# Kernel tuning notes

Hardware: AMD Instinct MI355X
Metric: run time of the kernel (lower is better)

The kernel has to match this reference:

```python
import jax, jax.numpy as jnp
import numpy as np

N = 50000   # nodes
E = 600000  # edges per edge_index
G = 64      # graphs in batch
H = 128     # hidden_neurons == n_node_features
EPS = 1e-12 # F.normalize eps


def sage(x, edge, Wl, bl, Wr, norm):
    # PyG SAGEConv (aggr='mean'): out_i = lin_l(mean_{j->i} x_j) + lin_r(x_i)
    src, dst = edge[0], edge[1]
    s = jax.ops.segment_sum(x[src], dst, num_segments=N)          # [N,H]
    cnt = jax.ops.segment_sum(jnp.ones((edge.shape[1],), x.dtype), dst, num_segments=N)
    agg = s / jnp.maximum(cnt, 1.0)[:, None]
    out = agg @ Wl + bl + x @ Wr
    if norm:  # F.normalize(out, p=2, dim=-1)
        n = jnp.linalg.norm(out, axis=-1, keepdims=True)
        out = out / jnp.maximum(n, EPS)
    return out


def setup_inputs() -> dict:
    key = jax.random.key(0)
    ks = jax.random.split(key, 40)
    sc = 1.0 / np.sqrt(H)
    d = {}
    d["x"] = jax.random.normal(ks[0], (N, H), jnp.float32)
    d["eic"] = jax.random.randint(ks[1], (2, E), 0, N, dtype=jnp.int32)
    d["eid"] = jax.random.randint(ks[2], (2, E), 0, N, dtype=jnp.int32)
    d["eit"] = jax.random.randint(ks[3], (2, E), 0, N, dtype=jnp.int32)
    d["batch"] = jnp.sort(jax.random.randint(ks[4], (N,), 0, G, dtype=jnp.int32))
    i = 5
    for c in ["c1", "c2", "c3", "c4", "c5"]:
        d[c + "_Wl"] = jax.random.normal(ks[i], (H, H), jnp.float32) * sc; i += 1
        d[c + "_bl"] = jnp.zeros((H,), jnp.float32)
        d[c + "_Wr"] = jax.random.normal(ks[i], (H, H), jnp.float32) * sc; i += 1
    d["l0_W"] = jax.random.normal(ks[i], (H, H), jnp.float32) * sc; i += 1
    d["l0_b"] = jnp.zeros((H,), jnp.float32)
    d["l1_W"] = jax.random.normal(ks[i], (H, H), jnp.float32) * sc; i += 1
    d["l1_b"] = jnp.zeros((H,), jnp.float32)
    d["head_W"] = jax.random.normal(ks[i], (H, 1), jnp.float32) * sc; i += 1
    d["head_b"] = jnp.zeros((1,), jnp.float32)
    return d


def reference(x, eic, eid, eit, batch,
              c1_Wl, c1_bl, c1_Wr, c2_Wl, c2_bl, c2_Wr, c3_Wl, c3_bl, c3_Wr,
              c4_Wl, c4_bl, c4_Wr, c5_Wl, c5_bl, c5_Wr,
              l0_W, l0_b, l1_W, l1_b, head_W, head_b):
    h = sage(x, eid, c1_Wl, c1_bl, c1_Wr, True)
    for _ in range(2):  # it_b4_dest, shared conv2 weights
        h = sage(h, eic, c2_Wl, c2_bl, c2_Wr, True)
    h = sage(h, eit, c3_Wl, c3_bl, c3_Wr, False)  # conv3 normalize=False
    h = sage(h, eid, c4_Wl, c4_bl, c4_Wr, True)
    for _ in range(2):  # it_aft_dest, shared conv5 weights
        h = sage(h, eic, c5_Wl, c5_bl, c5_Wr, True)
    g = jax.ops.segment_sum(h, batch, num_segments=G)  # global_add_pool -> [G,H]
    g = jax.nn.relu(g @ l0_W + l0_b)
    g = jax.nn.relu(g @ l1_W + l1_b)
    return g @ head_W + head_b  # [G,1]
```

## Files before the change

kernel.cpp:

```cpp
#include <hip/hip_runtime.h>
#include <hip/hip_bf16.h>


constexpr int N_NODES = 50000;
constexpr int NE      = 600000;
constexpr int H       = 128;
constexpr int NG      = 64;
constexpr int N3      = 3 * N_NODES;

constexpr int NB   = (N3 + 1023) >> 10;
constexpr int EPB  = 2048;
constexpr int BPS  = (NE + EPB - 1) / EPB;
constexpr int CAP2 = 19456;

typedef __attribute__((ext_vector_type(8))) short short8;
typedef __attribute__((ext_vector_type(4))) float f32x4;

__device__ __forceinline__ ushort f2bf(float f) {
    uint x = __float_as_uint(f);
    return (ushort)((x + 0x7FFFu + ((x >> 16) & 1u)) >> 16);
}
__device__ __forceinline__ float bf2f(ushort u) {
    return __uint_as_float(((uint)u) << 16);
}


__global__ __launch_bounds__(256) void k_bucketize(
    const int* __restrict__ e0, const int* __restrict__ e1,
    const int* __restrict__ e2, int* __restrict__ gcnt,
    int* __restrict__ rcnt, int2* __restrict__ bucket) {
    __shared__ int hist[NB];
    __shared__ int basearr[NB];
    __shared__ int cur[NB];
    __shared__ int gposs[NB];
    __shared__ int2 stage[EPB];
    __shared__ int dstoff[EPB];

    int t = threadIdx.x;
    int s = blockIdx.x / BPS;
    int w = blockIdx.x - s * BPS;
    const int* ep = (s == 0 ? e0 : (s == 1 ? e1 : e2));
    int eBase = w * EPB;
    int m = NE - eBase;
    if (m > EPB) m = EPB;

    for (int i = t; i < NB; i += 256) hist[i] = 0;
    __syncthreads();

    int myk[EPB / 256], mys[EPB / 256];
#pragma unroll
    for (int k = 0; k < EPB / 256; ++k) {
        int i = t + 256 * k;
        if (i < m) {
            int d   = ep[NE + eBase + i];
            int src = ep[eBase + i];
            int key = s * N_NODES + d;
            myk[k] = key; mys[k] = src;
            atomicAdd(&hist[key >> 10], 1);
        } else {
            myk[k] = -1;
        }
    }
    __syncthreads();

    if (t == 0) {
        int run = 0;
        for (int b = 0; b < NB; ++b) { basearr[b] = run; run += hist[b]; }
    }
    __syncthreads();

    if (t < NB) {
        int h = hist[t];
        int p = (h + 7) & ~7;
        gposs[t] = p ? atomicAdd(&gcnt[t], p) : 0;
        if (h) atomicAdd(&rcnt[t], h);
        cur[t] = 0;
    }
    __syncthreads();

#pragma unroll
    for (int k = 0; k < EPB / 256; ++k) {
        if (myk[k] >= 0) {
            int b  = myk[k] >> 10;
            int sl = atomicAdd(&cur[b], 1);
            int p  = basearr[b] + sl;
            stage[p]  = make_int2(myk[k], mys[k]);
            dstoff[p] = b * CAP2 + gposs[b] + sl;
        }
    }
    __syncthreads();

    for (int i = t; i < m; i += 256) bucket[dstoff[i]] = stage[i];
    for (int i = t; i < NB * 8; i += 256) {
        int b = i >> 3, j = i & 7;
        int h = hist[b];
        int p = (h + 7) & ~7;
        if (h + j < p)
            bucket[(size_t)b * CAP2 + gposs[b] + h + j] = make_int2(-1, 0);
    }
}


__global__ __launch_bounds__(512) void k_scatter2(const int2* __restrict__ bucket,
                                                  const int* __restrict__ gcnt,
                                                  const int* __restrict__ rcnt,
                                                  int* __restrict__ ptr,
                                                  int* __restrict__ adj) {
    int b = blockIdx.x;
    int base = b << 10;
    int nk = N3 - base;
    if (nk > 1024) nk = 1024;
    __shared__ int lh[1024];
    __shared__ int lsum[512];
    __shared__ int lfill[1024];
    __shared__ int bb;
    int t = threadIdx.x;

    int rv = (t < NB) ? rcnt[t] : 0;
    lsum[t] = rv;
    __syncthreads();
    for (int off = 1; off < 512; off <<= 1) {
        int u = (t >= off) ? lsum[t - off] : 0;
        __syncthreads();
        if (t >= off) lsum[t] += u;
        __syncthreads();
    }
    if (t == b) bb = lsum[t] - rv;
    if (b == 0 && t == 0) ptr[N3] = 3 * NE;
    for (int i = t; i < 1024; i += 512) lh[i] = 0;
    __syncthreads();

    int c = gcnt[b];
    const int2* seg = bucket + (size_t)b * CAP2;
    for (int i = t; i < c; i += 512) {
        int k = seg[i].x;
        if (k >= 0) atomicAdd(&lh[k - base], 1);
    }
    __syncthreads();
    int v0 = lh[t * 2], v1 = lh[t * 2 + 1];
    int ts = v0 + v1;
    lsum[t] = ts;
    __syncthreads();
    for (int off = 1; off < 512; off <<= 1) {
        int u = (t >= off) ? lsum[t - off] : 0;
        __syncthreads();
        if (t >= off) lsum[t] += u;
        __syncthreads();
    }
    int ex = lsum[t] - ts + bb;
    int e0 = ex, e1 = ex + v0;
    if (t * 2     < nk) { ptr[base + t * 2]     = e0; lfill[t * 2]     = e0; }
    if (t * 2 + 1 < nk) { ptr[base + t * 2 + 1] = e1; lfill[t * 2 + 1] = e1; }
    __syncthreads();
    for (int i = t; i < c; i += 512) {
        int2 ed = seg[i];
        if (ed.x >= 0) {
            int pos = atomicAdd(&lfill[ed.x - base], 1);
            adj[pos] = ed.y;
        }
    }
}


__global__ void k_prep(int* __restrict__ zmem,
                       const float* W0l, const float* W0r, const float* W1l,
                       const float* W1r, const float* W2l, const float* W2r,
                       const float* W3l, const float* W3r, const float* W4l,
                       const float* W4r, ushort* __restrict__ Bpk) {
    int bid = blockIdx.x;
    int t   = threadIdx.x;
    if (bid < 640) {
        int idx = bid * 256 + t;
        if (idx >= 5 * 32768) return;
        int c = idx >> 15, r = idx & 32767;
        const float* Wl = (c == 0 ? W0l : c == 1 ? W1l : c == 2 ? W2l : c == 3 ? W3l : W4l);
        const float* Wr = (c == 0 ? W0r : c == 1 ? W1r : c == 2 ? W2r : c == 3 ? W3r : W4r);
        int n = r & 255, k = r >> 8;
        float w = (n < H) ? Wl[k * H + n] : Wr[k * H + (n - H)];
        int q = k >> 5, g = (k >> 3) & 3, j = k & 7;
        int off = ((q * 4 + g) * 256 + n) * 8 + j;
        ushort h = f2bf(w);
        ushort* bh = Bpk + (size_t)c * 65536;
        bh[off]         = h;
        bh[32768 + off] = f2bf(w - bf2f(h));
        return;
    }
    int tid = (bid - 640) * 256 + t;
    if (tid < NG * H + 2 * NB) zmem[tid] = 0;
}


__global__ __launch_bounds__(256) void k_gemm0(
    const float* __restrict__ x,
    const ushort* __restrict__ Bh, const ushort* __restrict__ Bl,
    ushort* __restrict__ z, ushort* __restrict__ yb) {
    __shared__ ushort Ash[2][64][136];
    int t = threadIdx.x;
    int rowBase = blockIdx.x * 64;
    {
        int row = t >> 2;
        int cs  = (t & 3) * 32;
        int grow = rowBase + row;
        if (grow > N_NODES - 1) grow = N_NODES - 1;
        const float4* src = (const float4*)(x + (size_t)grow * H + cs);
        ushort* dh = &Ash[0][row][cs];
        ushort* dl = &Ash[1][row][cs];
#pragma unroll
        for (int i = 0; i < 8; ++i) {
            float4 v = src[i];
            ushort4 hh, ll;
            hh.x = f2bf(v.x); ll.x = f2bf(v.x - bf2f(hh.x));
            hh.y = f2bf(v.y); ll.y = f2bf(v.y - bf2f(hh.y));
            hh.z = f2bf(v.z); ll.z = f2bf(v.z - bf2f(hh.z));
            hh.w = f2bf(v.w); ll.w = f2bf(v.w - bf2f(hh.w));
            *(ushort4*)(dh + i * 4) = hh;
            *(ushort4*)(dl + i * 4) = ll;
        }
    }
    __syncthreads();

    int wave = t >> 6, lane = t & 63;
    int m16 = lane & 15, q4 = lane >> 4;
    int n0 = wave * 64;

    f32x4 acc[4][4];
#pragma unroll
    for (int r = 0; r < 4; ++r)
#pragma unroll
        for (int c = 0; c < 4; ++c) {
            acc[r][c][0] = 0.f; acc[r][c][1] = 0.f;
            acc[r][c][2] = 0.f; acc[r][c][3] = 0.f;
        }

    for (int q = 0; q < 4; ++q) {
        short8 bh_[4], bl_[4], ah_[4], al_[4];
#pragma unroll
        for (int c = 0; c < 4; ++c) {
            int boff = ((q * 4 + q4) * 256 + n0 + c * 16 + m16) * 8;
            bh_[c] = *(const short8*)(Bh + boff);
            bl_[c] = *(const short8*)(Bl + boff);
        }
#pragma unroll
        for (int r = 0; r < 4; ++r) {
            ah_[r] = *(const short8*)&Ash[0][r * 16 + m16][q * 32 + q4 * 8];
            al_[r] = *(const short8*)&Ash[1][r * 16 + m16][q * 32 + q4 * 8];
        }
#pragma unroll
        for (int r = 0; r < 4; ++r)
#pragma unroll
            for (int c = 0; c < 4; ++c) {
                acc[r][c] = __builtin_amdgcn_mfma_f32_16x16x32_bf16(
                    ah_[r], bh_[c], acc[r][c], 0, 0, 0);
                acc[r][c] = __builtin_amdgcn_mfma_f32_16x16x32_bf16(
                    ah_[r], bl_[c], acc[r][c], 0, 0, 0);
                acc[r][c] = __builtin_amdgcn_mfma_f32_16x16x32_bf16(
                    al_[r], bh_[c], acc[r][c], 0, 0, 0);
            }
    }

#pragma unroll
    for (int r = 0; r < 4; ++r)
#pragma unroll
        for (int c = 0; c < 4; ++c) {
            int col = n0 + c * 16 + m16;
            ushort* op = (col < H) ? (z + col) : (yb + (col - H));
#pragma unroll
            for (int j = 0; j < 4; ++j) {
                int gr = rowBase + r * 16 + q4 * 4 + j;
                if (gr < N_NODES) op[(size_t)gr * H] = f2bf(acc[r][c][j]);
            }
        }
}


__global__ __launch_bounds__(512, 6) void k_fused2(
    const ushort* __restrict__ zin, const ushort* __restrict__ yin,
    ushort* __restrict__ zout, ushort* __restrict__ yout,
    const int* __restrict__ ptr, const int* __restrict__ adj,
    const float* __restrict__ bl,
    const ushort* __restrict__ Bh, const ushort* __restrict__ Blw,
    int norm) {
    __shared__ ushort Ash[2][32][136];
    int t = threadIdx.x;
    int rowBase = blockIdx.x * 32;
    int sl  = t & 15;
    int row = t >> 4;

    {
        int node = rowBase + row;
        if (node > N_NODES - 1) node = N_NODES - 1;
        int beg = ptr[node], end = ptr[node + 1];
        int deg = end - beg;
        const ushort* zrow = zin + sl * 8;
        float a[8];
#pragma unroll
        for (int k = 0; k < 8; ++k) a[k] = 0.f;

        for (int base = 0; base < deg; base += 16) {
            int m = deg - base;
            if (m > 16) m = 16;
            int idx = (sl < m) ? adj[beg + base + sl] : 0;
#pragma unroll
            for (int half = 0; half < 2; ++half) {
                int mh = m - half * 8;
                if (mh <= 0) continue;
                if (mh > 8) mh = 8;
                int hb = half * 8;
                short8 v[8];
#pragma unroll
                for (int jj = 0; jj < 8; ++jj) {
                    int nj = __shfl(idx, hb + jj, 16);
                    if (jj < mh) v[jj] = *(const short8*)(zrow + (size_t)nj * H);
                }
                if (mh == 8) {
#pragma unroll
                    for (int k = 0; k < 8; ++k)
                        a[k] += ((bf2f((ushort)v[0][k]) + bf2f((ushort)v[1][k])) +
                                 (bf2f((ushort)v[2][k]) + bf2f((ushort)v[3][k]))) +
                                ((bf2f((ushort)v[4][k]) + bf2f((ushort)v[5][k])) +
                                 (bf2f((ushort)v[6][k]) + bf2f((ushort)v[7][k])));
                } else if (mh >= 4) {
#pragma unroll
                    for (int k = 0; k < 8; ++k)
                        a[k] += (bf2f((ushort)v[0][k]) + bf2f((ushort)v[1][k])) +
                                (bf2f((ushort)v[2][k]) + bf2f((ushort)v[3][k]));
                    if (mh > 4) {
#pragma unroll
                        for (int k = 0; k < 8; ++k) a[k] += bf2f((ushort)v[4][k]);
                    }
                    if (mh > 5) {
#pragma unroll
                        for (int k = 0; k < 8; ++k) a[k] += bf2f((ushort)v[5][k]);
                    }
                    if (mh > 6) {
#pragma unroll
                        for (int k = 0; k < 8; ++k) a[k] += bf2f((ushort)v[6][k]);
                    }
                } else {
                    if (mh > 0) {
#pragma unroll
                        for (int k = 0; k < 8; ++k) a[k] += bf2f((ushort)v[0][k]);
                    }
                    if (mh > 1) {
#pragma unroll
                        for (int k = 0; k < 8; ++k) a[k] += bf2f((ushort)v[1][k]);
                    }
                    if (mh > 2) {
#pragma unroll
                        for (int k = 0; k < 8; ++k) a[k] += bf2f((ushort)v[2][k]);
                    }
                }
            }
        }

        float inv = 1.0f / (float)(deg > 1 ? deg : 1);
        short8 yv = *(const short8*)(yin + (size_t)node * H + sl * 8);
        float4 bva = *(const float4*)(bl + sl * 8);
        float4 bvb = *(const float4*)(bl + sl * 8 + 4);
        float vv[8];
        vv[0] = a[0] * inv + bva.x + bf2f((ushort)yv[0]);
        vv[1] = a[1] * inv + bva.y + bf2f((ushort)yv[1]);
        vv[2] = a[2] * inv + bva.z + bf2f((ushort)yv[2]);
        vv[3] = a[3] * inv + bva.w + bf2f((ushort)yv[3]);
        vv[4] = a[4] * inv + bvb.x + bf2f((ushort)yv[4]);
        vv[5] = a[5] * inv + bvb.y + bf2f((ushort)yv[5]);
        vv[6] = a[6] * inv + bvb.z + bf2f((ushort)yv[6]);
        vv[7] = a[7] * inv + bvb.w + bf2f((ushort)yv[7]);
        if (norm) {
            float ss = 0.f;
#pragma unroll
            for (int k = 0; k < 8; ++k) ss += vv[k] * vv[k];
#pragma unroll
            for (int mm = 1; mm < 16; mm <<= 1) ss += __shfl_xor(ss, mm, 16);
            float n2 = 1.0f / fmaxf(sqrtf(ss), 1e-12f);
#pragma unroll
            for (int k = 0; k < 8; ++k) vv[k] *= n2;
        }
        short8 ho, lo8;
#pragma unroll
        for (int k = 0; k < 8; ++k) {
            ushort hh = f2bf(vv[k]);
            ho[k]  = (short)hh;
            lo8[k] = (short)f2bf(vv[k] - bf2f(hh));
        }
        *(short8*)&Ash[0][row][sl * 8] = ho;
        *(short8*)&Ash[1][row][sl * 8] = lo8;
    }
    __syncthreads();

    int wave = t >> 6, lane = t & 63;
    int m16 = lane & 15, q4 = lane >> 4;
    int wr = wave & 1;
    int n0 = (wave >> 1) * 64;

    f32x4 acc[4];
#pragma unroll
    for (int c = 0; c < 4; ++c) {
        acc[c][0] = 0.f; acc[c][1] = 0.f; acc[c][2] = 0.f; acc[c][3] = 0.f;
    }

    for (int q = 0; q < 4; ++q) {
        short8 ah_ = *(const short8*)&Ash[0][wr * 16 + m16][q * 32 + q4 * 8];
        short8 al_ = *(const short8*)&Ash[1][wr * 16 + m16][q * 32 + q4 * 8];
#pragma unroll
        for (int c = 0; c < 4; ++c) {
            int boff = ((q * 4 + q4) * 256 + n0 + c * 16 + m16) * 8;
            short8 bh_ = *(const short8*)(Bh + boff);
            short8 bl_ = *(const short8*)(Blw + boff);
            acc[c] = __builtin_amdgcn_mfma_f32_16x16x32_bf16(ah_, bh_, acc[c], 0, 0, 0);
            acc[c] = __builtin_amdgcn_mfma_f32_16x16x32_bf16(ah_, bl_, acc[c], 0, 0, 0);
            acc[c] = __builtin_amdgcn_mfma_f32_16x16x32_bf16(al_, bh_, acc[c], 0, 0, 0);
        }
    }

#pragma unroll
    for (int c = 0; c < 4; ++c) {
        int col = n0 + c * 16 + m16;
        ushort* op = (col < H) ? (zout + col) : (yout + (col - H));
#pragma unroll
        for (int j = 0; j < 4; ++j) {
            int gr = rowBase + wr * 16 + q4 * 4 + j;
            if (gr < N_NODES) op[(size_t)gr * H] = f2bf(acc[c][j]);
        }
    }
}


__global__ __launch_bounds__(256, 8) void k_aggpool(
    const ushort* __restrict__ z, const ushort* __restrict__ yb,
    const int* __restrict__ ptr, const int* __restrict__ adj,
    const float* __restrict__ bl, const int* __restrict__ batch,
    float* __restrict__ g) {
    __shared__ float accs[16][H];
    __shared__ int gfirst;
    int t = threadIdx.x;
    int node0 = blockIdx.x * 16;
    int gtid = blockIdx.x * 256 + t;
    int node = gtid >> 4;
    int sl   = t & 15;
    for (int i = t; i < 16 * H; i += 256) ((float*)accs)[i] = 0.f;
    if (t == 0) gfirst = batch[node0 < N_NODES ? node0 : N_NODES - 1];
    __syncthreads();

    if (node < N_NODES) {
        int beg = ptr[node], end = ptr[node + 1];
        int deg = end - beg;
        const ushort* zrow = z + sl * 8;
        float a[8];
#pragma unroll
        for (int k = 0; k < 8; ++k) a[k] = 0.f;

        for (int base = 0; base < deg; base += 16) {
            int m = deg - base;
            if (m > 16) m = 16;
            int idx = (sl < m) ? adj[beg + base + sl] : 0;
#pragma unroll
            for (int half = 0; half < 2; ++half) {
                int mh = m - half * 8;
                if (mh <= 0) continue;
                if (mh > 8) mh = 8;
                int hb = half * 8;
                short8 v[8];
#pragma unroll
                for (int jj = 0; jj < 8; ++jj) {
                    int nj = __shfl(idx, hb + jj, 16);
                    if (jj < mh) v[jj] = *(const short8*)(zrow + (size_t)nj * H);
                }
                if (mh == 8) {
#pragma unroll
                    for (int k = 0; k < 8; ++k)
                        a[k] += ((bf2f((ushort)v[0][k]) + bf2f((ushort)v[1][k])) +
                                 (bf2f((ushort)v[2][k]) + bf2f((ushort)v[3][k]))) +
                                ((bf2f((ushort)v[4][k]) + bf2f((ushort)v[5][k])) +
                                 (bf2f((ushort)v[6][k]) + bf2f((ushort)v[7][k])));
                } else if (mh >= 4) {
#pragma unroll
                    for (int k = 0; k < 8; ++k)
                        a[k] += (bf2f((ushort)v[0][k]) + bf2f((ushort)v[1][k])) +
                                (bf2f((ushort)v[2][k]) + bf2f((ushort)v[3][k]));
                    if (mh > 4) {
#pragma unroll
                        for (int k = 0; k < 8; ++k) a[k] += bf2f((ushort)v[4][k]);
                    }
                    if (mh > 5) {
#pragma unroll
                        for (int k = 0; k < 8; ++k) a[k] += bf2f((ushort)v[5][k]);
                    }
                    if (mh > 6) {
#pragma unroll
                        for (int k = 0; k < 8; ++k) a[k] += bf2f((ushort)v[6][k]);
                    }
                } else {
                    if (mh > 0) {
#pragma unroll
                        for (int k = 0; k < 8; ++k) a[k] += bf2f((ushort)v[0][k]);
                    }
                    if (mh > 1) {
#pragma unroll
                        for (int k = 0; k < 8; ++k) a[k] += bf2f((ushort)v[1][k]);
                    }
                    if (mh > 2) {
#pragma unroll
                        for (int k = 0; k < 8; ++k) a[k] += bf2f((ushort)v[2][k]);
                    }
                }
            }
        }

        float inv = 1.0f / (float)(deg > 1 ? deg : 1);
        short8 yv = *(const short8*)(yb + (size_t)node * H + sl * 8);
        float4 bva = *(const float4*)(bl + sl * 8);
        float4 bvb = *(const float4*)(bl + sl * 8 + 4);
        float vv[8];
        vv[0] = a[0] * inv + bva.x + bf2f((ushort)yv[0]);
        vv[1] = a[1] * inv + bva.y + bf2f((ushort)yv[1]);
        vv[2] = a[2] * inv + bva.z + bf2f((ushort)yv[2]);
        vv[3] = a[3] * inv + bva.w + bf2f((ushort)yv[3]);
        vv[4] = a[4] * inv + bvb.x + bf2f((ushort)yv[4]);
        vv[5] = a[5] * inv + bvb.y + bf2f((ushort)yv[5]);
        vv[6] = a[6] * inv + bvb.z + bf2f((ushort)yv[6]);
        vv[7] = a[7] * inv + bvb.w + bf2f((ushort)yv[7]);
        {
            float ss = 0.f;
#pragma unroll
            for (int k = 0; k < 8; ++k) ss += vv[k] * vv[k];
#pragma unroll
            for (int mm = 1; mm < 16; mm <<= 1) ss += __shfl_xor(ss, mm, 16);
            float n2 = 1.0f / fmaxf(sqrtf(ss), 1e-12f);
#pragma unroll
            for (int k = 0; k < 8; ++k) vv[k] *= n2;
        }
        int gl = batch[node] - gfirst;
        if (gl < 16) {
#pragma unroll
            for (int k = 0; k < 8; ++k) atomicAdd(&accs[gl][sl * 8 + k], vv[k]);
        } else {
#pragma unroll
            for (int k = 0; k < 8; ++k)
                atomicAdd(&g[(size_t)batch[node] * H + sl * 8 + k], vv[k]);
        }
    }
    __syncthreads();

    int lastnode = node0 + 15;
    if (lastnode > N_NODES - 1) lastnode = N_NODES - 1;
    int nsl = batch[lastnode] - gfirst + 1;
    if (nsl > 16) nsl = 16;
    for (int i = t; i < nsl * H; i += 256)
        atomicAdd(&g[(size_t)(gfirst + i / H) * H + (i % H)], accs[i / H][i % H]);
}


__global__ void k_mlp(const float* __restrict__ g, const float* __restrict__ W0,
                      const float* __restrict__ b0, const float* __restrict__ W1,
                      const float* __restrict__ b1, const float* __restrict__ Wh,
                      const float* __restrict__ bh, float* __restrict__ out) {
    int gi = blockIdx.x;
    int t  = threadIdx.x;
    __shared__ float buf0[H];
    __shared__ float buf1[H];
    __shared__ float red[2];

    float acc = b0[t];
    for (int k = 0; k < H; ++k) acc += g[gi * H + k] * W0[k * H + t];
    buf0[t] = fmaxf(acc, 0.f);
    __syncthreads();

    acc = b1[t];
    for (int k = 0; k < H; ++k) acc += buf0[k] * W1[k * H + t];
    buf1[t] = fmaxf(acc, 0.f);
    __syncthreads();

    float p = buf1[t] * Wh[t];
    for (int m = 1; m < 64; m <<= 1) p += __shfl_xor(p, m, 64);
    if ((t & 63) == 0) red[t >> 6] = p;
    __syncthreads();
    if (t == 0) out[gi] = red[0] + red[1] + bh[0];
}


extern "C" void kernel_launch(void* const* d_in, const int* in_sizes, int n_in,
                              void* d_out, int out_size, void* d_ws, size_t ws_size,
                              hipStream_t stream) {
    const float* x     = (const float*)d_in[0];
    const int*   eic   = (const int*)d_in[1];
    const int*   eid   = (const int*)d_in[2];
    const int*   eit   = (const int*)d_in[3];
    const int*   batch = (const int*)d_in[4];
    const float* cW[5][3];
    for (int c = 0; c < 5; ++c) {
        cW[c][0] = (const float*)d_in[5 + c * 3 + 0];
        cW[c][1] = (const float*)d_in[5 + c * 3 + 1];
        cW[c][2] = (const float*)d_in[5 + c * 3 + 2];
    }
    const float* l0_W = (const float*)d_in[20];
    const float* l0_b = (const float*)d_in[21];
    const float* l1_W = (const float*)d_in[22];
    const float* l1_b = (const float*)d_in[23];
    const float* hd_W = (const float*)d_in[24];
    const float* hd_b = (const float*)d_in[25];
    float* outp = (float*)d_out;

    const size_t NH = (size_t)N_NODES * H;
    ushort* zb0 = (ushort*)d_ws;
    ushort* yb0 = zb0 + NH;
    ushort* zb1 = yb0 + NH;
    ushort* yb1 = zb1 + NH;
    ushort* Bpk = yb1 + NH;
    float*  gbuf = (float*)(Bpk + 5 * 2 * 32768);
    int* gcnt = (int*)(gbuf + (size_t)NG * H);
    int* rcnt = gcnt + NB;
    int* ptr_all = rcnt + NB;
    int* adj_all = ptr_all + (N3 + 1);
    int2* bucket = (int2*)zb0;

    dim3 b256(256);

    k_prep<<<dim3(640 + 34), b256, 0, stream>>>(
        (int*)gbuf,
        cW[0][0], cW[0][2], cW[1][0], cW[1][2], cW[2][0], cW[2][2],
        cW[3][0], cW[3][2], cW[4][0], cW[4][2], Bpk);

    k_bucketize<<<dim3(3 * BPS), b256, 0, stream>>>(eic, eid, eit, gcnt, rcnt, bucket);
    k_scatter2<<<dim3(NB), dim3(512), 0, stream>>>(bucket, gcnt, rcnt, ptr_all, adj_all);

    const int L_set[7]  = {1, 0, 0, 2, 1, 0, 0};
    const int L_conv[7] = {0, 1, 1, 2, 3, 4, 4};
    const int L_norm[7] = {1, 1, 1, 0, 1, 1, 1};

    dim3 gGemm((N_NODES + 63) / 64);
    dim3 gFused((N_NODES + 31) / 32);
    dim3 gAggP((N_NODES * 16 + 255) / 256);

    k_gemm0<<<gGemm, b256, 0, stream>>>(x, Bpk + (size_t)L_conv[0] * 65536,
                                        Bpk + (size_t)L_conv[0] * 65536 + 32768,
                                        zb0, yb0);

    for (int L = 0; L < 6; ++L) {
        ushort* zi = (L & 1) ? zb1 : zb0;
        ushort* yi = (L & 1) ? yb1 : yb0;
        ushort* zo = (L & 1) ? zb0 : zb1;
        ushort* yo = (L & 1) ? yb0 : yb1;
        const ushort* Bh = Bpk + (size_t)L_conv[L + 1] * 65536;
        const ushort* Bl = Bh + 32768;
        k_fused2<<<gFused, dim3(512), 0, stream>>>(zi, yi, zo, yo,
                                                   ptr_all + L_set[L] * N_NODES,
                                                   adj_all, cW[L_conv[L]][1], Bh, Bl,
                                                   L_norm[L]);
    }

    k_aggpool<<<gAggP, b256, 0, stream>>>(zb0, yb0, ptr_all + L_set[6] * N_NODES,
                                          adj_all, cW[L_conv[6]][1], batch, gbuf);

    k_mlp<<<dim3(NG), dim3(H), 0, stream>>>(gbuf, l0_W, l0_b, l1_W, l1_b, hd_W, hd_b,
                                            outp);
}
```

Baseline: 471.7 us.

## Replace shared-memory atomics in pooling with segmented per-column reduction

In the aggregation-plus-pool kernel, each node's normalized row is now written directly into a shared slot, along with its graph id. After that, 128 threads each walk the 16 rows for one column and emit one global atomic per graph segment. This removes the zero-init pass, the extra barrier, and the shared-memory atomics, relying on the batch array being sorted. Separately, the fused conv kernel's launch bounds minimum blocks per CU is raised from 6 to 8, which may force register spilling. If every node in a block is out of range, the kernel adds zero to g[-1] out of bounds; with N=50000 and 16 nodes per block that block never occurs.

```diff
diff --git a/kernel.cpp b/kernel.cpp
--- a/kernel.cpp
+++ b/kernel.cpp
@@ -273,7 +273,7 @@
 }
 
 
-__global__ __launch_bounds__(512, 6) void k_fused2(
+__global__ __launch_bounds__(512, 8) void k_fused2(
     const ushort* __restrict__ zin, const ushort* __restrict__ yin,
     ushort* __restrict__ zout, ushort* __restrict__ yout,
     const int* __restrict__ ptr, const int* __restrict__ adj,
@@ -432,15 +432,12 @@
     const float* __restrict__ bl, const int* __restrict__ batch,
     float* __restrict__ g) {
     __shared__ float accs[16][H];
-    __shared__ int gfirst;
+    __shared__ int gid[16];
     int t = threadIdx.x;
-    int node0 = blockIdx.x * 16;
     int gtid = blockIdx.x * 256 + t;
     int node = gtid >> 4;
     int sl   = t & 15;
-    for (int i = t; i < 16 * H; i += 256) ((float*)accs)[i] = 0.f;
-    if (t == 0) gfirst = batch[node0 < N_NODES ? node0 : N_NODES - 1];
-    __syncthreads();
+    int nib  = t >> 4;
 
     if (node < N_NODES) {
         int beg = ptr[node], end = ptr[node + 1];
@@ -530,24 +527,29 @@
 #pragma unroll
             for (int k = 0; k < 8; ++k) vv[k] *= n2;
         }
-        int gl = batch[node] - gfirst;
-        if (gl < 16) {
-#pragma unroll
-            for (int k = 0; k < 8; ++k) atomicAdd(&accs[gl][sl * 8 + k], vv[k]);
-        } else {
-#pragma unroll
-            for (int k = 0; k < 8; ++k)
-                atomicAdd(&g[(size_t)batch[node] * H + sl * 8 + k], vv[k]);
-        }
-    }
-    __syncthreads();
-
-    int lastnode = node0 + 15;
-    if (lastnode > N_NODES - 1) lastnode = N_NODES - 1;
-    int nsl = batch[lastnode] - gfirst + 1;
-    if (nsl > 16) nsl = 16;
-    for (int i = t; i < nsl * H; i += 256)
-        atomicAdd(&g[(size_t)(gfirst + i / H) * H + (i % H)], accs[i / H][i % H]);
+#pragma unroll
+        for (int k = 0; k < 8; ++k) accs[nib][sl * 8 + k] = vv[k];
+        if (sl == 0) gid[nib] = batch[node];
+    } else {
+        if (sl == 0) gid[nib] = -1;
+    }
+    __syncthreads();
+
+    if (t < H) {
+        int col = t;
+        float run = 0.f;
+        int cur = gid[0];
+        for (int i = 0; i < 16; ++i) {
+            int gg = gid[i];
+            if (gg < 0) break;
+            if (gg != cur) {
+                atomicAdd(&g[(size_t)cur * H + col], run);
+                run = 0.f; cur = gg;
+            }
+            run += accs[i][col];
+        }
+        atomicAdd(&g[(size_t)cur * H + col], run);
+    }
 }
 
 
```

New measurement: 455.6 us. 1.04x faster.
